# Kernel optimization log

Hardware: AMD Instinct MI355X
Metric: run time of the kernel (lower is better)

## Reference

```python
import jax, jax.numpy as jnp
import numpy as np

NEG_SLOPE = 0.2  # LeakyReLU slope
PAD = 1          # padding for all 3x3 convs (kernel_size // 2)
K = 9            # 3x3 deformable kernel taps


def _conv2d(x, w, b):
    # x: (B,Cin,H,W), w: (Cout,Cin,3,3) -> (B,Cout,H,W), stride 1, SAME pad
    y = jax.lax.conv_general_dilated(x, w, (1, 1), 'SAME',
                                     dimension_numbers=('NCHW', 'OIHW', 'NCHW'))
    return y + b[None, :, None, None]


def _leaky(x):
    return jnp.where(x >= 0, x, NEG_SLOPE * x)


def _deform_conv(x, offset, w, b):
    # torchvision DeformConv2d, kernel 3x3, stride 1, pad 1, no modulation.
    # x: (B,C,H,W); offset: (B, 2*K, H, W) ordered (dy,dx) per tap; w: (O,C,3,3)
    B, C, H, W = x.shape
    O = w.shape[0]
    off = offset.reshape(B, K, 2, H, W)
    ks = jnp.arange(K)
    ky = (ks // 3).astype(x.dtype)
    kx = (ks % 3).astype(x.dtype)
    iy = jnp.arange(H, dtype=x.dtype)
    ix = jnp.arange(W, dtype=x.dtype)
    # sampling locations: out_pos + tap_pos - pad + learned offset  -> (B,K,H,W)
    py = iy[None, None, :, None] + ky[None, :, None, None] - PAD + off[:, :, 0]
    px = ix[None, None, None, :] + kx[None, :, None, None] - PAD + off[:, :, 1]

    y0 = jnp.floor(py)
    x0 = jnp.floor(px)
    wy = py - y0
    wx = px - x0
    y0i = y0.astype(jnp.int32)
    x0i = x0.astype(jnp.int32)

    def gather(img, yi, xi):  # img: (C,H,W); yi,xi: (K,H,W) -> (C,K,H,W)
        return img[:, yi, xi]
    vgather = jax.vmap(gather)  # over batch

    def corner(yi, xi, wgt):
        valid = (yi >= 0) & (yi < H) & (xi >= 0) & (xi < W)
        yc = jnp.clip(yi, 0, H - 1)
        xc = jnp.clip(xi, 0, W - 1)
        v = vgather(x, yc, xc)  # (B,C,K,H,W)
        return v * (wgt * valid.astype(x.dtype))[:, None]

    val = (corner(y0i, x0i, (1 - wy) * (1 - wx))
           + corner(y0i, x0i + 1, (1 - wy) * wx)
           + corner(y0i + 1, x0i, wy * (1 - wx))
           + corner(y0i + 1, x0i + 1, wy * wx))  # (B,C,K,H,W)
    out = jnp.einsum('bckhw,ock->bohw', val, w.reshape(O, C, K))
    return out + b[None, :, None, None]


def _stage(x, cw, cb, ow, ob, dw, db):
    h = _leaky(_conv2d(x, cw, cb))      # plain conv + LeakyReLU
    off = _conv2d(h, ow, ob)            # offset prediction (18 channels)
    return _leaky(_deform_conv(h, off, dw, db))


def setup_inputs() -> dict:
    key = jax.random.key(0)
    keys = iter(jax.random.split(key, 32))

    def nrm(shape, scale):
        return jax.random.normal(next(keys), shape, jnp.float32) * scale

    inp = {'x': jax.random.normal(next(keys), (4, 64, 128, 128), jnp.float32)}
    specs = [(64, 128), (128, 128), (128, 64)]
    for i, (ci, co) in enumerate(specs, 1):
        inp[f's{i}_cw'] = nrm((co, ci, 3, 3), (ci * 9) ** -0.5)
        inp[f's{i}_cb'] = jnp.zeros((co,), jnp.float32)
        inp[f's{i}_ow'] = nrm((18, co, 3, 3), 0.1 * (co * 9) ** -0.5)  # small offsets
        inp[f's{i}_ob'] = jnp.zeros((18,), jnp.float32)
        inp[f's{i}_dw'] = nrm((co, co, 3, 3), (co * 9) ** -0.5)
        inp[f's{i}_db'] = jnp.zeros((co,), jnp.float32)
    return inp


def reference(x,
              s1_cw, s1_cb, s1_ow, s1_ob, s1_dw, s1_db,
              s2_cw, s2_cb, s2_ow, s2_ob, s2_dw, s2_db,
              s3_cw, s3_cb, s3_ow, s3_ob, s3_dw, s3_db):
    x = _stage(x, s1_cw, s1_cb, s1_ow, s1_ob, s1_dw, s1_db)
    x = _stage(x, s2_cw, s2_cb, s2_ow, s2_ob, s2_dw, s2_db)
    x = _stage(x, s3_cw, s3_cb, s3_ow, s3_ob, s3_dw, s3_db)
    return x
```

## Files before the change

### kernel.cpp

```cpp
#include <hip/hip_runtime.h>
#include <hip/hip_bf16.h>

#define HW 128
#define HW2 16384
#define NEG 0.2f

typedef __attribute__((ext_vector_type(8))) short short8;
typedef __attribute__((ext_vector_type(4))) float f32x4;
typedef __attribute__((ext_vector_type(2))) float f32x2;
typedef __attribute__((ext_vector_type(16))) float f32x16;

__device__ __forceinline__ float lrelu(float v) { return v >= 0.f ? v : NEG * v; }
__device__ __forceinline__ unsigned short f2bf(float f) {
    unsigned int u = __float_as_uint(f);
    u = (u + 0x7fffu + ((u >> 16) & 1u)) >> 16;
    return (unsigned short)u;
}
__device__ __forceinline__ unsigned int pk2(float a, float b) {
    __hip_bfloat162 h = __float22bfloat162_rn(float2{a, b});
    return *(unsigned int*)&h;
}
__device__ __forceinline__ float2 upk(unsigned int u) {
    return float2{__uint_as_float(u << 16), __uint_as_float(u & 0xffff0000u)};
}
__device__ __forceinline__ f32x2 upkv(unsigned int u) {
    f32x2 r;
    r.x = __uint_as_float(u << 16);
    r.y = __uint_as_float(u & 0xffff0000u);
    return r;
}

struct WSeg { const float* s; unsigned short* d; int K9; int NMT; int validM; int n; int mode; };
struct WArgs { WSeg seg[9]; };

__global__ void wrepack_kernel(WArgs a)
{
    const WSeg sg = a.seg[blockIdx.y];
    int i = blockIdx.x * 256 + threadIdx.x;
    if (i >= sg.n) return;
    int cl = i & 7, lane = (i >> 3) & 63;
    int rest = i >> 9;
    unsigned short v = 0;
    if (sg.mode == 0) {
        int mt = rest % sg.NMT, gs = rest / sg.NMT;
        int st = gs % 3, g = gs / 3;
        int quad = lane >> 4, l15 = lane & 15;
        int co = mt * 16 + l15, tap = st * 4 + quad;
        if (tap < 9 && co < sg.validM)
            v = f2bf(sg.s[(size_t)co * sg.K9 + (g * 8 + cl) * 9 + tap]);
    } else {
        int mt = rest % sg.NMT, kig = rest / sg.NMT;
        int ki = kig % 5, g = kig / 5;
        int hi = lane >> 5, l31 = lane & 31;
        int co = mt * 32 + l31, tap = ki * 2 + hi;
        if (tap < 9 && co < sg.validM)
            v = f2bf(sg.s[(size_t)co * sg.K9 + (g * 8 + cl) * 9 + tap]);
    }
    sg.d[i] = v;
}

template <int MTW, int SRCF>
__global__ __launch_bounds__(256, 4) void fused_conv(
    const void* __restrict__ actv, const unsigned short* __restrict__ wpad,
    const float* __restrict__ bias, unsigned short* __restrict__ outb,
    float* __restrict__ outf, int Cin, int Cout, int mode)
{
    constexpr int PB = 136 * 16;
    constexpr int SMB = 64 * 136 * 2;
    __shared__ char smem[SMB];
    unsigned short* Es = (unsigned short*)smem;

    const int t = threadIdx.x;
    const int tile = blockIdx.x, b = blockIdx.z;
    const int lane = t & 63, wv = t >> 6, quad = lane >> 4, l15 = lane & 15;
    const int y0 = (tile >> 2) * 2, x0 = (tile & 3) * 32;
    const int ngrp = Cin >> 3;
    const int NSTR = (Cout >> 4) * 512;

    const bool sok = lane < 34;
    const int gy = y0 - 1 + wv, gx = x0 - 1 + lane;
    const bool pok = sok && gy >= 0 && gy < HW && gx >= 0 && gx < HW;
    const int gp = pok ? gy * HW + gx : 0;
    const int slot = wv * 34 + lane;

    const float* actf = (const float*)actv;
    const unsigned short* acth = (const unsigned short*)actv;
    const size_t bofs = (size_t)b * Cin * HW2;

    int baddr[3][4];
#pragma unroll
    for (int st = 0; st < 3; ++st) {
        int tap = st * 4 + quad; tap = tap > 8 ? 8 : tap;
        int ky = (tap * 11) >> 5, kx = tap - 3 * ky;
#pragma unroll
        for (int nt = 0; nt < 4; ++nt) {
            int p = nt * 16 + l15, ly = p >> 5, lx = p & 31;
            baddr[st][nt] = ((ly + ky) * 34 + lx + kx) * 16;
        }
    }
    size_t abase[MTW];
#pragma unroll
    for (int m = 0; m < MTW; ++m)
        abase[m] = (size_t)((wv * MTW + m) * 512 + lane * 8);

    f32x4 acc[MTW][4];
#pragma unroll
    for (int m = 0; m < MTW; ++m)
#pragma unroll
        for (int nt = 0; nt < 4; ++nt) acc[m][nt] = (f32x4)(0.f);

    auto load_grp = [&](int g) -> uint4 {
        uint4 u; u.x = u.y = u.z = u.w = 0;
        if (!pok) return u;
        if (SRCF == 1) {
            u = *(const uint4*)(acth + bofs + ((size_t)g * HW2 + gp) * 8);
        } else {
            const float* pl = actf + bofs + (size_t)(g * 8) * HW2 + gp;
            float v0 = pl[0], v1 = pl[HW2], v2 = pl[2 * HW2], v3 = pl[3 * HW2];
            float v4 = pl[4 * HW2], v5 = pl[5 * HW2], v6 = pl[6 * HW2], v7 = pl[7 * HW2];
            u.x = pk2(v0, v1); u.y = pk2(v2, v3);
            u.z = pk2(v4, v5); u.w = pk2(v6, v7);
        }
        return u;
    };

    short8 apre[MTW][3];
    auto loadA = [&](int g) {
#pragma unroll
        for (int st = 0; st < 3; ++st)
#pragma unroll
            for (int m = 0; m < MTW; ++m)
                apre[m][st] = *(const short8*)(wpad + (size_t)(g * 3 + st) * NSTR + abase[m]);
    };

    uint4 cur = load_grp(0);
    if (sok) *(uint4*)(smem + slot * 16) = cur;
    loadA(0);
    if (ngrp > 1) cur = load_grp(1);
    __syncthreads();

    for (int g = 0; g < ngrp; ++g) {
        char* pb = smem + (g & 1) * PB;
#pragma unroll
        for (int st = 0; st < 3; ++st) {
            short8 bfr[4];
#pragma unroll
            for (int nt = 0; nt < 4; ++nt)
                bfr[nt] = *(const short8*)(pb + baddr[st][nt]);
#pragma unroll
            for (int m = 0; m < MTW; ++m) {
                short8 a = apre[m][st];
#pragma unroll
                for (int nt = 0; nt < 4; ++nt)
                    acc[m][nt] = __builtin_amdgcn_mfma_f32_16x16x32_bf16(
                        a, bfr[nt], acc[m][nt], 0, 0, 0);
            }
        }
        if (g + 1 < ngrp) {
            if (sok) *(uint4*)(smem + ((g + 1) & 1) * PB + slot * 16) = cur;
            loadA(g + 1);
            if (g + 2 < ngrp) cur = load_grp(g + 2);
        }
        __syncthreads();
    }

    if (mode == 0) {
        constexpr int ESTR = 136;
#pragma unroll
        for (int m = 0; m < MTW; ++m) {
            int cb = (wv * MTW + m) * 16;
#pragma unroll
            for (int nt = 0; nt < 4; ++nt) {
                int px = nt * 16 + l15;
                int co = cb + quad * 4;
                unsigned int u0 = pk2(lrelu(acc[m][nt][0] + bias[co]),
                                      lrelu(acc[m][nt][1] + bias[co + 1]));
                unsigned int u1 = pk2(lrelu(acc[m][nt][2] + bias[co + 2]),
                                      lrelu(acc[m][nt][3] + bias[co + 3]));
                uint2 u; u.x = u0; u.y = u1;
                *(uint2*)&Es[px * ESTR + co] = u;
            }
        }
        __syncthreads();
        const int ng8 = Cout >> 3;
        unsigned short* ob = outb + (size_t)b * Cout * HW2;
        for (int tt = t; tt < 64 * ng8; tt += 256) {
            int cg = tt >> 6, px = tt & 63;
            int gp2 = (y0 + (px >> 5)) * HW + x0 + (px & 31);
            *(uint4*)(ob + ((size_t)cg * HW2 + gp2) * 8) =
                *(const uint4*)&Es[px * ESTR + cg * 8];
        }
    } else {
        float* of = outf + (size_t)b * 18 * HW2;
#pragma unroll
        for (int m = 0; m < MTW; ++m) {
            int cb = (wv * MTW + m) * 16;
#pragma unroll
            for (int nt = 0; nt < 4; ++nt) {
                int px = nt * 16 + l15;
                int gp2 = (y0 + (px >> 5)) * HW + x0 + (px & 31);
#pragma unroll
                for (int r = 0; r < 4; ++r) {
                    int co = cb + quad * 4 + r;
                    if (co < 18)
                        of[(size_t)co * HW2 + gp2] = acc[m][nt][r] + bias[co];
                }
            }
        }
    }
}

template <int NMT, int NT>
__global__ __launch_bounds__(256, 4) void fused_deform(
    const unsigned short* __restrict__ acth,
    const unsigned short* __restrict__ woff, const float* __restrict__ obias,
    const unsigned short* __restrict__ wpad, const float* __restrict__ bias,
    unsigned short* __restrict__ outb, float* __restrict__ outf,
    int Cin, int Cout, int mode)
{
    constexpr int PATW = 43, PATR = 8, PATP = PATR * PATW;
    constexpr int CSTR = 88;
    constexpr int PB = PATP * 16;
    constexpr int CB = 64 * CSTR * 2;
    constexpr int SMB = 2 * PB + 2 * CB;
    constexpr int OPB = 136 * 16;
    __shared__ char smem[SMB];
    unsigned short* Es = (unsigned short*)smem;

    const int t = threadIdx.x;
    const int tile = blockIdx.x, b = blockIdx.z;
    const int lane = t & 63, wv = t >> 6, quad = lane >> 4, l15 = lane & 15;
    const int l31 = lane & 31, hi = lane >> 5;
    const int y0 = (tile >> 2) * 2, x0 = (tile & 3) * 32;
    const int ngrp = Cin >> 3;
    const int NSTR2 = NMT * 512;
    const int py0 = y0 - 3, px0 = x0 - 5;
    const size_t bofs = (size_t)b * Cin * HW2;

    for (int i = t; i < 128; i += 256) {
        int bu = i >> 6, p = i & 63;
        uint4 z; z.x = z.y = z.z = z.w = 0;
        *(uint4*)(smem + 2 * PB + bu * CB + (p * CSTR + 72) * 2) = z;
    }

    {
        float* offbuf = (float*)(smem + 2 * OPB);
        const bool asok = lane < 34;
        const int agy = y0 - 1 + wv, agx = x0 - 1 + lane;
        const bool apok = asok && agy >= 0 && agy < HW && agx >= 0 && agx < HW;
        const int agp = apok ? agy * HW + agx : 0;
        const int aslot = wv * 34 + lane;

        const int mtile = wv & 1, npair = wv >> 1;
        int obad[3][2];
#pragma unroll
        for (int st = 0; st < 3; ++st) {
            int tap = st * 4 + quad; tap = tap > 8 ? 8 : tap;
            int ky = (tap * 11) >> 5, kx = tap - 3 * ky;
#pragma unroll
            for (int nn = 0; nn < 2; ++nn) {
                int p = (2 * npair + nn) * 16 + l15, ly = p >> 5, lx = p & 31;
                obad[st][nn] = ((ly + ky) * 34 + lx + kx) * 16;
            }
        }
        const size_t oa0 = (size_t)(mtile * 512 + lane * 8);

        f32x4 oacc[2];
        oacc[0] = (f32x4)(0.f); oacc[1] = (f32x4)(0.f);
        short8 oapre[3];
        auto loadAO = [&](int g) {
#pragma unroll
            for (int st = 0; st < 3; ++st)
                oapre[st] = *(const short8*)(woff + (size_t)(g * 3 + st) * 1024 + oa0);
        };
        auto load_g = [&](int g) -> uint4 {
            uint4 u; u.x = u.y = u.z = u.w = 0;
            if (apok) u = *(const uint4*)(acth + bofs + ((size_t)g * HW2 + agp) * 8);
            return u;
        };

        uint4 cur = load_g(0);
        if (asok) *(uint4*)(smem + aslot * 16) = cur;
        loadAO(0);
        if (ngrp > 1) cur = load_g(1);
        __syncthreads();

        for (int g = 0; g < ngrp; ++g) {
            const char* pb = smem + (g & 1) * OPB;
#pragma unroll
            for (int st = 0; st < 3; ++st) {
                short8 a = oapre[st];
#pragma unroll
                for (int nn = 0; nn < 2; ++nn) {
                    short8 bf = *(const short8*)(pb + obad[st][nn]);
                    oacc[nn] = __builtin_amdgcn_mfma_f32_16x16x32_bf16(
                        a, bf, oacc[nn], 0, 0, 0);
                }
            }
            if (g + 1 < ngrp) {
                if (asok) *(uint4*)(smem + ((g + 1) & 1) * OPB + aslot * 16) = cur;
                loadAO(g + 1);
                if (g + 2 < ngrp) cur = load_g(g + 2);
            }
            __syncthreads();
        }

        {
            int co0 = mtile * 16 + quad * 4;
            if (co0 < 18) {
#pragma unroll
                for (int nn = 0; nn < 2; ++nn) {
                    int px = (2 * npair + nn) * 16 + l15;
#pragma unroll
                    for (int r = 0; r < 4; ++r)
                        if (co0 + r < 18)
                            offbuf[px * 20 + co0 + r] = oacc[nn][r] + obias[co0 + r];
                }
            }
        }
        __syncthreads();
    }
    const float* offbuf = (const float*)(smem + 2 * OPB);

    float w00[3], w01[3], w10[3], w11[3];
    int pbase[3], csad[3], svalid[3];
    int allin = 1;
    {
#pragma unroll
        for (int s = 0; s < 3; ++s) {
            int task = t + s * 256;
            svalid[s] = task < 576;
            int task2 = svalid[s] ? task : 0;
            int p = task2 / 9, k = task2 - 9 * p;
            int yy = y0 + (p >> 5), xx = x0 + (p & 31);
            float2 dd = *(const float2*)(offbuf + p * 20 + 2 * k);
            float dy = dd.x, dx = dd.y;
            float py = (float)(yy + k / 3 - 1) + dy;
            float px = (float)(xx + k % 3 - 1) + dx;
            float fy = floorf(py), fx = floorf(px);
            float wy = py - fy, wx = px - fx;
            int iy = (int)fy, ix = (int)fx;
            w00[s] = (1.f - wy) * (1.f - wx);
            w01[s] = (1.f - wy) * wx;
            w10[s] = wy * (1.f - wx);
            w11[s] = wy * wx;
            pbase[s] = ((iy - py0) * PATW + (ix - px0)) * 16;
            csad[s] = (p * CSTR + k * 8) * 2;
            bool ip = iy >= py0 && iy + 1 <= py0 + (PATR - 1)
                   && ix >= px0 && ix + 1 <= px0 + (PATW - 1);
            if (!ip) allin = 0;
        }
    }
    const int fast = __syncthreads_and(allin);

    const int s0 = wv * 86 + lane;
    const int r0 = s0 / PATW, c0_ = s0 - PATW * r0;
    const int gy0_ = py0 + r0, gx0_ = px0 + c0_;
    const bool ok0 = gy0_ >= 0 && gy0_ < HW && gx0_ >= 0 && gx0_ < HW;
    const int go0 = ok0 ? gy0_ * HW + gx0_ : 0;
    const bool has1 = lane < 22;
    const int s1 = wv * 86 + 64 + lane;
    const int r1 = s1 / PATW, c1_ = s1 - PATW * r1;
    const int gy1_ = py0 + r1, gx1_ = px0 + c1_;
    const bool ok1 = has1 && gy1_ >= 0 && gy1_ < HW && gx1_ >= 0 && gx1_ < HW;
    const int go1 = ok1 ? gy1_ * HW + gx1_ : 0;

    const int mt0 = (NT == 2) ? wv : (wv >> 1);
    const size_t abase2 = (size_t)(mt0 * 512 + lane * 8);
    int bbn[NT];
#pragma unroll
    for (int n = 0; n < NT; ++n) {
        int nh = (NT == 2) ? n : (wv & 1);
        bbn[n] = (nh * 32 + l31) * (CSTR * 2) + hi * 16;
    }

    f32x16 acc2[NT];
#pragma unroll
    for (int n = 0; n < NT; ++n) acc2[n] = (f32x16)(0.f);

    short8 apre[5];
    auto loadA = [&](int g) {
#pragma unroll
        for (int ki = 0; ki < 5; ++ki)
            apre[ki] = *(const short8*)(
                wpad + (size_t)(g * 5 + ki) * NSTR2 + abase2);
    };

    auto mfma32 = [&](const char* cs) {
#pragma unroll
        for (int ki = 0; ki < 5; ++ki) {
            short8 bf[NT];
#pragma unroll
            for (int n = 0; n < NT; ++n)
                bf[n] = *(const short8*)(cs + bbn[n] + ki * 32);
#pragma unroll
            for (int n = 0; n < NT; ++n)
                acc2[n] = __builtin_amdgcn_mfma_f32_32x32x16_bf16(
                    apre[ki], bf[n], acc2[n], 0, 0, 0);
        }
    };

    if (fast) {
        uint4 u0, u1;
        u0.x = u0.y = u0.z = u0.w = 0; u1 = u0;
        if (ok0) u0 = *(const uint4*)(acth + bofs + (size_t)go0 * 8);
        if (ok1) u1 = *(const uint4*)(acth + bofs + (size_t)go1 * 8);
        *(uint4*)(smem + s0 * 16) = u0;
        if (has1) *(uint4*)(smem + s1 * 16) = u1;
        if (ngrp > 1) {
            u0.x = u0.y = u0.z = u0.w = 0; u1 = u0;
            if (ok0) u0 = *(const uint4*)(acth + bofs + ((size_t)HW2 + go0) * 8);
            if (ok1) u1 = *(const uint4*)(acth + bofs + ((size_t)HW2 + go1) * 8);
        }
        __syncthreads();

        for (int g = 0; g < ngrp; ++g) {
            const char* pb = smem + (g & 1) * PB;
            char* csW = smem + 2 * PB + (g & 1) * CB;

            if (g > 0)
                mfma32(smem + 2 * PB + ((g - 1) & 1) * CB);

#pragma unroll
            for (int s = 0; s < 3; ++s) {
                if (!svalid[s]) continue;
                const char* base = pb + pbase[s];
                uint4 c00 = *(const uint4*)base;
                uint4 c01 = *(const uint4*)(base + 16);
                uint4 c10 = *(const uint4*)(base + PATW * 16);
                uint4 c11 = *(const uint4*)(base + PATW * 16 + 16);
                f32x2 vw0 = (f32x2)(w00[s]), vw1 = (f32x2)(w01[s]);
                f32x2 vw2 = (f32x2)(w10[s]), vw3 = (f32x2)(w11[s]);
                f32x2 a0 = vw0 * upkv(c00.x) + vw1 * upkv(c01.x)
                         + vw2 * upkv(c10.x) + vw3 * upkv(c11.x);
                f32x2 a1 = vw0 * upkv(c00.y) + vw1 * upkv(c01.y)
                         + vw2 * upkv(c10.y) + vw3 * upkv(c11.y);
                f32x2 a2 = vw0 * upkv(c00.z) + vw1 * upkv(c01.z)
                         + vw2 * upkv(c10.z) + vw3 * upkv(c11.z);
                f32x2 a3 = vw0 * upkv(c00.w) + vw1 * upkv(c01.w)
                         + vw2 * upkv(c10.w) + vw3 * upkv(c11.w);
                uint4 ou;
                ou.x = pk2(a0.x, a0.y); ou.y = pk2(a1.x, a1.y);
                ou.z = pk2(a2.x, a2.y); ou.w = pk2(a3.x, a3.y);
                *(uint4*)(csW + csad[s]) = ou;
            }

            if (g + 1 < ngrp) {
                char* pn = smem + ((g + 1) & 1) * PB;
                *(uint4*)(pn + s0 * 16) = u0;
                if (has1) *(uint4*)(pn + s1 * 16) = u1;
            }
            loadA(g);
            if (g + 2 < ngrp) {
                u0.x = u0.y = u0.z = u0.w = 0; u1 = u0;
                if (ok0) u0 = *(const uint4*)(acth + bofs +
                                              ((size_t)(g + 2) * HW2 + go0) * 8);
                if (ok1) u1 = *(const uint4*)(acth + bofs +
                                              ((size_t)(g + 2) * HW2 + go1) * 8);
            }
            __syncthreads();
        }
        mfma32(smem + 2 * PB + ((ngrp - 1) & 1) * CB);
    } else {
        char* csW = smem + 2 * PB;
        for (int g = 0; g < ngrp; ++g) {
            const unsigned short* gb = acth + bofs + (size_t)g * HW2 * 8;
#pragma unroll
            for (int s = 0; s < 3; ++s) {
                if (!svalid[s]) continue;
                int task = t + s * 256;
                int p = task / 9, k = task - 9 * p;
                int yy = y0 + (p >> 5), xx = x0 + (p & 31);
                float2 dd = *(const float2*)(offbuf + p * 20 + 2 * k);
                float dy = dd.x, dx = dd.y;
                float py = (float)(yy + k / 3 - 1) + dy;
                float px = (float)(xx + k % 3 - 1) + dx;
                float fy = floorf(py), fx = floorf(px);
                float wy = py - fy, wx = px - fx;
                int iy = (int)fy, ix = (int)fx;
                float f0 = 0, f1 = 0, f2 = 0, f3 = 0, f4 = 0, f5 = 0, f6 = 0, f7 = 0;
#pragma unroll
                for (int q = 0; q < 4; ++q) {
                    int ddy = q >> 1, ddx = q & 1;
                    int sy = iy + ddy, sx = ix + ddx;
                    float w = (ddy ? wy : 1.f - wy) * (ddx ? wx : 1.f - wx);
                    if (sy < 0 || sy >= HW || sx < 0 || sx >= HW) w = 0.f;
                    int cy = min(max(sy, 0), HW - 1), cx = min(max(sx, 0), HW - 1);
                    uint4 c = *(const uint4*)(gb + (size_t)(cy * HW + cx) * 8);
                    float2 p0 = upk(c.x), p1 = upk(c.y), p2 = upk(c.z), p3 = upk(c.w);
                    f0 += w * p0.x; f1 += w * p0.y; f2 += w * p1.x; f3 += w * p1.y;
                    f4 += w * p2.x; f5 += w * p2.y; f6 += w * p3.x; f7 += w * p3.y;
                }
                uint4 ou;
                ou.x = pk2(f0, f1); ou.y = pk2(f2, f3);
                ou.z = pk2(f4, f5); ou.w = pk2(f6, f7);
                *(uint4*)(csW + csad[s]) = ou;
            }
            __syncthreads();
            loadA(g);
            mfma32(csW);
            __syncthreads();
        }
    }

    __syncthreads();
    if (mode == 0) {
        constexpr int ESTR = 136;
        int mtb = mt0 * 32;
#pragma unroll
        for (int n = 0; n < NT; ++n) {
            int px2 = ((NT == 2) ? n : (wv & 1)) * 32 + l31;
#pragma unroll
            for (int q = 0; q < 4; ++q) {
                int co = mtb + q * 8 + hi * 4;
                unsigned int u0 = pk2(lrelu(acc2[n][q * 4 + 0] + bias[co]),
                                      lrelu(acc2[n][q * 4 + 1] + bias[co + 1]));
                unsigned int u1 = pk2(lrelu(acc2[n][q * 4 + 2] + bias[co + 2]),
                                      lrelu(acc2[n][q * 4 + 3] + bias[co + 3]));
                uint2 u; u.x = u0; u.y = u1;
                *(uint2*)&Es[px2 * ESTR + co] = u;
            }
        }
        __syncthreads();
        const int ng8 = Cout >> 3;
        unsigned short* ob = outb + (size_t)b * Cout * HW2;
        for (int tt = t; tt < 64 * ng8; tt += 256) {
            int cg = tt >> 6, px = tt & 63;
            int gp2 = (y0 + (px >> 5)) * HW + x0 + (px & 31);
            *(uint4*)(ob + ((size_t)cg * HW2 + gp2) * 8) =
                *(const uint4*)&Es[px * ESTR + cg * 8];
        }
    } else {
        float* of = outf + (size_t)b * Cout * HW2;
        int mtb = mt0 * 32;
#pragma unroll
        for (int n = 0; n < NT; ++n) {
            int px2 = ((NT == 2) ? n : (wv & 1)) * 32 + l31;
            int gp2 = (y0 + (px2 >> 5)) * HW + x0 + (px2 & 31);
#pragma unroll
            for (int q = 0; q < 4; ++q) {
                int co = mtb + q * 8 + hi * 4;
#pragma unroll
                for (int rr = 0; rr < 4; ++rr)
                    of[(size_t)(co + rr) * HW2 + gp2] =
                        lrelu(acc2[n][q * 4 + rr] + bias[co + rr]);
            }
        }
    }
}

extern "C" void kernel_launch(void* const* d_in, const int* in_sizes, int n_in,
                              void* d_out, int out_size, void* d_ws,
                              size_t ws_size, hipStream_t stream)
{
    const float* x = (const float*)d_in[0];
    const float* p[18];
    for (int i = 0; i < 18; ++i) p[i] = (const float*)d_in[1 + i];

    char* ws = (char*)d_ws;
    unsigned short* A1 = (unsigned short*)ws;
    unsigned short* A2 = (unsigned short*)(ws + 16777216);
    unsigned short* WB = (unsigned short*)(ws + 38273024);

    unsigned short* Wc1 = WB;
    unsigned short* Wo1 = Wc1 + 98304;
    unsigned short* Wd1 = Wo1 + 49152;
    unsigned short* Wc2 = Wd1 + 163840;
    unsigned short* Wo2 = Wc2 + 196608;
    unsigned short* Wd2 = Wo2 + 49152;
    unsigned short* Wc3 = Wd2 + 163840;
    unsigned short* Wo3 = Wc3 + 98304;
    unsigned short* Wd3 = Wo3 + 24576;

    WArgs wa;
    wa.seg[0] = {p[0],  Wc1,  576, 8, 128,  98304, 0};
    wa.seg[1] = {p[2],  Wo1, 1152, 2,  18,  49152, 0};
    wa.seg[2] = {p[4],  Wd1, 1152, 4, 128, 163840, 1};
    wa.seg[3] = {p[6],  Wc2, 1152, 8, 128, 196608, 0};
    wa.seg[4] = {p[8],  Wo2, 1152, 2,  18,  49152, 0};
    wa.seg[5] = {p[10], Wd2, 1152, 4, 128, 163840, 1};
    wa.seg[6] = {p[12], Wc3, 1152, 4,  64,  98304, 0};
    wa.seg[7] = {p[14], Wo3,  576, 2,  18,  24576, 0};
    wa.seg[8] = {p[16], Wd3,  576, 2,  64,  40960, 1};
    wrepack_kernel<<<dim3(768, 9), 256, 0, stream>>>(wa);

    dim3 g(256, 1, 4);
    fused_conv<2, 0><<<g, 256, 0, stream>>>(x, Wc1, p[1], A1, nullptr, 64, 128, 0);
    fused_deform<4, 2><<<g, 256, 0, stream>>>(A1, Wo1, p[3], Wd1, p[5], A2, nullptr, 128, 128, 0);
    fused_conv<2, 1><<<g, 256, 0, stream>>>(A2, Wc2, p[7], A1, nullptr, 128, 128, 0);
    fused_deform<4, 2><<<g, 256, 0, stream>>>(A1, Wo2, p[9], Wd2, p[11], A2, nullptr, 128, 128, 0);
    fused_conv<1, 1><<<g, 256, 0, stream>>>(A2, Wc3, p[13], A1, nullptr, 128, 64, 0);
    fused_deform<2, 1><<<g, 256, 0, stream>>>(A1, Wo3, p[15], Wd3, p[17], nullptr, (float*)d_out, 64, 64, 1);
}
```

Baseline: 287.4 us.

## Switch plain conv kernels to 32x32x16 MFMA with 2-tap K packing

Rewrites fused_conv to use 32x32x16 bf16 MFMA instructions. Each instruction covers two taps of an 8-channel group, so 5 tap-pairs replace the 3 four-tap steps, and the weights are repacked in the deform kernel's mode-1 layout. The goal is to cut instruction count and LDS B-fragment reads per FLOP, and to shrink the padded weight buffers (the 9 taps now pad to 10 instead of 12). The unused offset-output mode is dropped. In exchange each lane holds larger accumulators and the epilogue index mapping changes.

```diff
diff --git a/kernel.cpp b/kernel.cpp
--- a/kernel.cpp
+++ b/kernel.cpp
@@ -59,11 +59,11 @@
     sg.d[i] = v;
 }
 
-template <int MTW, int SRCF>
+template <int NMT, int NT, int SRCF>
 __global__ __launch_bounds__(256, 4) void fused_conv(
     const void* __restrict__ actv, const unsigned short* __restrict__ wpad,
     const float* __restrict__ bias, unsigned short* __restrict__ outb,
-    float* __restrict__ outf, int Cin, int Cout, int mode)
+    int Cin, int Cout)
 {
     constexpr int PB = 136 * 16;
     constexpr int SMB = 64 * 136 * 2;
@@ -72,10 +72,11 @@
 
     const int t = threadIdx.x;
     const int tile = blockIdx.x, b = blockIdx.z;
-    const int lane = t & 63, wv = t >> 6, quad = lane >> 4, l15 = lane & 15;
+    const int lane = t & 63, wv = t >> 6;
+    const int l31 = lane & 31, hi = lane >> 5;
     const int y0 = (tile >> 2) * 2, x0 = (tile & 3) * 32;
     const int ngrp = Cin >> 3;
-    const int NSTR = (Cout >> 4) * 512;
+    const int NSTR2 = NMT * 512;
 
     const bool sok = lane < 34;
     const int gy = y0 - 1 + wv, gx = x0 - 1 + lane;
@@ -87,27 +88,23 @@
     const unsigned short* acth = (const unsigned short*)actv;
     const size_t bofs = (size_t)b * Cin * HW2;
 
-    int baddr[3][4];
-#pragma unroll
-    for (int st = 0; st < 3; ++st) {
-        int tap = st * 4 + quad; tap = tap > 8 ? 8 : tap;
+    int baddr2[5][NT];
+#pragma unroll
+    for (int ki = 0; ki < 5; ++ki) {
+        int tap = ki * 2 + hi; tap = tap > 8 ? 8 : tap;
         int ky = (tap * 11) >> 5, kx = tap - 3 * ky;
 #pragma unroll
-        for (int nt = 0; nt < 4; ++nt) {
-            int p = nt * 16 + l15, ly = p >> 5, lx = p & 31;
-            baddr[st][nt] = ((ly + ky) * 34 + lx + kx) * 16;
-        }
-    }
-    size_t abase[MTW];
-#pragma unroll
-    for (int m = 0; m < MTW; ++m)
-        abase[m] = (size_t)((wv * MTW + m) * 512 + lane * 8);
-
-    f32x4 acc[MTW][4];
-#pragma unroll
-    for (int m = 0; m < MTW; ++m)
-#pragma unroll
-        for (int nt = 0; nt < 4; ++nt) acc[m][nt] = (f32x4)(0.f);
+        for (int n = 0; n < NT; ++n) {
+            int nh = (NT == 2) ? n : (wv & 1);
+            baddr2[ki][n] = ((nh + ky) * 34 + l31 + kx) * 16;
+        }
+    }
+    const int mt0 = (NT == 2) ? wv : (wv >> 1);
+    const size_t abase2 = (size_t)(mt0 * 512 + lane * 8);
+
+    f32x16 acc2[NT];
+#pragma unroll
+    for (int n = 0; n < NT; ++n) acc2[n] = (f32x16)(0.f);
 
     auto load_grp = [&](int g) -> uint4 {
         uint4 u; u.x = u.y = u.z = u.w = 0;
@@ -124,13 +121,12 @@
         return u;
     };
 
-    short8 apre[MTW][3];
+    short8 apre[5];
     auto loadA = [&](int g) {
 #pragma unroll
-        for (int st = 0; st < 3; ++st)
-#pragma unroll
-            for (int m = 0; m < MTW; ++m)
-                apre[m][st] = *(const short8*)(wpad + (size_t)(g * 3 + st) * NSTR + abase[m]);
+        for (int ki = 0; ki < 5; ++ki)
+            apre[ki] = *(const short8*)(
+                wpad + (size_t)(g * 5 + ki) * NSTR2 + abase2);
     };
 
     uint4 cur = load_grp(0);
@@ -142,19 +138,15 @@
     for (int g = 0; g < ngrp; ++g) {
         char* pb = smem + (g & 1) * PB;
 #pragma unroll
-        for (int st = 0; st < 3; ++st) {
-            short8 bfr[4];
-#pragma unroll
-            for (int nt = 0; nt < 4; ++nt)
-                bfr[nt] = *(const short8*)(pb + baddr[st][nt]);
-#pragma unroll
-            for (int m = 0; m < MTW; ++m) {
-                short8 a = apre[m][st];
-#pragma unroll
-                for (int nt = 0; nt < 4; ++nt)
-                    acc[m][nt] = __builtin_amdgcn_mfma_f32_16x16x32_bf16(
-                        a, bfr[nt], acc[m][nt], 0, 0, 0);
-            }
+        for (int ki = 0; ki < 5; ++ki) {
+            short8 bf[NT];
+#pragma unroll
+            for (int n = 0; n < NT; ++n)
+                bf[n] = *(const short8*)(pb + baddr2[ki][n]);
+#pragma unroll
+            for (int n = 0; n < NT; ++n)
+                acc2[n] = __builtin_amdgcn_mfma_f32_32x32x16_bf16(
+                    apre[ki], bf[n], acc2[n], 0, 0, 0);
         }
         if (g + 1 < ngrp) {
             if (sok) *(uint4*)(smem + ((g + 1) & 1) * PB + slot * 16) = cur;
@@ -164,21 +156,21 @@
         __syncthreads();
     }
 
-    if (mode == 0) {
+    {
         constexpr int ESTR = 136;
-#pragma unroll
-        for (int m = 0; m < MTW; ++m) {
-            int cb = (wv * MTW + m) * 16;
-#pragma unroll
-            for (int nt = 0; nt < 4; ++nt) {
-                int px = nt * 16 + l15;
-                int co = cb + quad * 4;
-                unsigned int u0 = pk2(lrelu(acc[m][nt][0] + bias[co]),
-                                      lrelu(acc[m][nt][1] + bias[co + 1]));
-                unsigned int u1 = pk2(lrelu(acc[m][nt][2] + bias[co + 2]),
-                                      lrelu(acc[m][nt][3] + bias[co + 3]));
+        int mtb = mt0 * 32;
+#pragma unroll
+        for (int n = 0; n < NT; ++n) {
+            int px2 = ((NT == 2) ? n : (wv & 1)) * 32 + l31;
+#pragma unroll
+            for (int q = 0; q < 4; ++q) {
+                int co = mtb + q * 8 + hi * 4;
+                unsigned int u0 = pk2(lrelu(acc2[n][q * 4 + 0] + bias[co]),
+                                      lrelu(acc2[n][q * 4 + 1] + bias[co + 1]));
+                unsigned int u1 = pk2(lrelu(acc2[n][q * 4 + 2] + bias[co + 2]),
+                                      lrelu(acc2[n][q * 4 + 3] + bias[co + 3]));
                 uint2 u; u.x = u0; u.y = u1;
-                *(uint2*)&Es[px * ESTR + co] = u;
+                *(uint2*)&Es[px2 * ESTR + co] = u;
             }
         }
         __syncthreads();
@@ -189,23 +181,6 @@
             int gp2 = (y0 + (px >> 5)) * HW + x0 + (px & 31);
             *(uint4*)(ob + ((size_t)cg * HW2 + gp2) * 8) =
                 *(const uint4*)&Es[px * ESTR + cg * 8];
-        }
-    } else {
-        float* of = outf + (size_t)b * 18 * HW2;
-#pragma unroll
-        for (int m = 0; m < MTW; ++m) {
-            int cb = (wv * MTW + m) * 16;
-#pragma unroll
-            for (int nt = 0; nt < 4; ++nt) {
-                int px = nt * 16 + l15;
-                int gp2 = (y0 + (px >> 5)) * HW + x0 + (px & 31);
-#pragma unroll
-                for (int r = 0; r < 4; ++r) {
-                    int co = cb + quad * 4 + r;
-                    if (co < 18)
-                        of[(size_t)co * HW2 + gp2] = acc[m][nt][r] + bias[co];
-                }
-            }
         }
     }
 }
@@ -563,32 +538,32 @@
     unsigned short* WB = (unsigned short*)(ws + 38273024);
 
     unsigned short* Wc1 = WB;
-    unsigned short* Wo1 = Wc1 + 98304;
+    unsigned short* Wo1 = Wc1 + 81920;
     unsigned short* Wd1 = Wo1 + 49152;
     unsigned short* Wc2 = Wd1 + 163840;
-    unsigned short* Wo2 = Wc2 + 196608;
+    unsigned short* Wo2 = Wc2 + 163840;
     unsigned short* Wd2 = Wo2 + 49152;
     unsigned short* Wc3 = Wd2 + 163840;
-    unsigned short* Wo3 = Wc3 + 98304;
+    unsigned short* Wo3 = Wc3 + 81920;
     unsigned short* Wd3 = Wo3 + 24576;
 
     WArgs wa;
-    wa.seg[0] = {p[0],  Wc1,  576, 8, 128,  98304, 0};
+    wa.seg[0] = {p[0],  Wc1,  576, 4, 128,  81920, 1};
     wa.seg[1] = {p[2],  Wo1, 1152, 2,  18,  49152, 0};
     wa.seg[2] = {p[4],  Wd1, 1152, 4, 128, 163840, 1};
-    wa.seg[3] = {p[6],  Wc2, 1152, 8, 128, 196608, 0};
+    wa.seg[3] = {p[6],  Wc2, 1152, 4, 128, 163840, 1};
     wa.seg[4] = {p[8],  Wo2, 1152, 2,  18,  49152, 0};
     wa.seg[5] = {p[10], Wd2, 1152, 4, 128, 163840, 1};
-    wa.seg[6] = {p[12], Wc3, 1152, 4,  64,  98304, 0};
+    wa.seg[6] = {p[12], Wc3, 1152, 2,  64,  81920, 1};
     wa.seg[7] = {p[14], Wo3,  576, 2,  18,  24576, 0};
     wa.seg[8] = {p[16], Wd3,  576, 2,  64,  40960, 1};
     wrepack_kernel<<<dim3(768, 9), 256, 0, stream>>>(wa);
 
     dim3 g(256, 1, 4);
-    fused_conv<2, 0><<<g, 256, 0, stream>>>(x, Wc1, p[1], A1, nullptr, 64, 128, 0);
+    fused_conv<4, 2, 0><<<g, 256, 0, stream>>>(x, Wc1, p[1], A1, 64, 128);
     fused_deform<4, 2><<<g, 256, 0, stream>>>(A1, Wo1, p[3], Wd1, p[5], A2, nullptr, 128, 128, 0);
-    fused_conv<2, 1><<<g, 256, 0, stream>>>(A2, Wc2, p[7], A1, nullptr, 128, 128, 0);
+    fused_conv<4, 2, 1><<<g, 256, 0, stream>>>(A2, Wc2, p[7], A1, 128, 128);
     fused_deform<4, 2><<<g, 256, 0, stream>>>(A1, Wo2, p[9], Wd2, p[11], A2, nullptr, 128, 128, 0);
-    fused_conv<1, 1><<<g, 256, 0, stream>>>(A2, Wc3, p[13], A1, nullptr, 128, 64, 0);
+    fused_conv<2, 1, 1><<<g, 256, 0, stream>>>(A2, Wc3, p[13], A1, 128, 64);
     fused_deform<2, 1><<<g, 256, 0, stream>>>(A1, Wo3, p[15], Wd3, p[17], nullptr, (float*)d_out, 64, 64, 1);
 }
```

Measured after the change: 295.8 us. +2.9%, slower.
